# Kernel tuning notes

Hardware: AMD Instinct MI355X
Metric: run time of the kernel (lower is better)

## Reference

```python
import jax, jax.numpy as jnp
import numpy as np

N_NODES = 50000
N_EDGES = 800000
D_IN = 96
D_OUT = 96
K_ORDER = 3


def setup_inputs() -> dict:
    key = jax.random.key(0)
    k1, k2, k3, k4, k5 = jax.random.split(key, 5)
    rows = jax.random.randint(k1, (N_EDGES,), 0, N_NODES, dtype=jnp.int64 if jax.config.jax_enable_x64 else jnp.int32)
    cols = jax.random.randint(k2, (N_EDGES,), 0, N_NODES, dtype=jnp.int64 if jax.config.jax_enable_x64 else jnp.int32)
    vals = jax.random.uniform(k3, (N_EDGES,), dtype=jnp.float32) * (1.0 / 16.0)  # ~sym-normalized weights
    H = jax.random.normal(k4, (N_NODES, D_IN), dtype=jnp.float32)
    W = jax.random.normal(k5, (D_IN, D_OUT), dtype=jnp.float32) * (1.0 / np.sqrt(D_IN))
    bias = jnp.zeros((D_OUT,), dtype=jnp.float32)
    return {"rows": rows, "cols": cols, "vals": vals, "H": H, "W": W, "bias": bias}


def reference(rows, cols, vals, H, W, bias):
    n = H.shape[0]

    def spmm(X):  # L @ X via gather-multiply-scatter over COO edges
        return jax.ops.segment_sum(vals[:, None] * X[cols], rows, num_segments=n)

    def ln_mm(X):  # (2L - I) @ X
        return 2.0 * spmm(X) - X

    # k = 0 term: T_0 = H
    H_out = H @ W
    # k = 1 term: T_1 = (2L - I) H  (differentiable, as in torch code)
    T_prev = H
    T_curr = ln_mm(H)
    H_out = H_out + T_curr @ W
    # k >= 2: recurrence computed under no_grad in the original -> stop_gradient
    for _ in range(2, K_ORDER + 1):
        T_next = jax.lax.stop_gradient(2.0 * ln_mm(T_curr) - T_prev)
        H_out = H_out + T_next @ W
        T_prev, T_curr = T_curr, T_next
    return H_out + bias
```

## Files before the change

### kernel.cpp

```cpp
#include <hip/hip_runtime.h>
#include <hip/hip_fp16.h>

#define NN 50000
#define NE 800000
#define D  96
#define NB_SCAN 196
#define N4 (NN * D / 4)
#define CB4 ((N4 + 255) / 256)
#define WFRAG_BLKS 5
#define EMAX (NE + 8 * NN)
#define EZ4  (EMAX / 4)
#define EZB  ((EZ4 + 255) / 256)

typedef unsigned int   uint32;
typedef unsigned short uint16;
typedef short  v8s __attribute__((ext_vector_type(8)));
typedef float  v4f __attribute__((ext_vector_type(4)));
typedef unsigned int v2u __attribute__((ext_vector_type(2)));
typedef unsigned int v4u __attribute__((ext_vector_type(4)));

__device__ inline uint16 f32_to_bf16(float f) {
    uint32 u = __float_as_uint(f);
    u += 0x7FFF + ((u >> 16) & 1);
    return (uint16)(u >> 16);
}

__device__ inline void u2f(v2u u, float& a, float& b, float& c, float& d) {
    a = __uint_as_float(u.x << 16);
    b = __uint_as_float(u.x & 0xFFFF0000u);
    c = __uint_as_float(u.y << 16);
    d = __uint_as_float(u.y & 0xFFFF0000u);
}

__device__ inline float f16_val(uint32 e) {
    __half_raw h; h.x = (uint16)(e >> 16);
    return __half2float(__half(h));
}

__device__ inline uint32 comb2(uint32 u1, uint32 u2, uint32 u3) {
    float a1 = __uint_as_float(u1 << 16), b1 = __uint_as_float(u1 & 0xFFFF0000u);
    float a2 = __uint_as_float(u2 << 16), b2 = __uint_as_float(u2 & 0xFFFF0000u);
    float a3 = __uint_as_float(u3 << 16), b3 = __uint_as_float(u3 & 0xFFFF0000u);
    float sa = 12.f * a1 - 40.f * a2 + 32.f * a3;
    float sb = 12.f * b1 - 40.f * b2 + 32.f * b3;
    return (uint32)f32_to_bf16(sa) | ((uint32)f32_to_bf16(sb) << 16);
}

__global__ void prep(const float4* __restrict__ H, ushort4* __restrict__ Hb,
                     const float* __restrict__ W, uint16* __restrict__ Wfrag,
                     int* __restrict__ counts, v4u* __restrict__ edges4) {
    int b = blockIdx.x;
    int t = threadIdx.x;
    if (b < CB4) {
        int i = b * 256 + t;
        if (i < N4) {
            float4 v = H[i];
            ushort4 o;
            o.x = f32_to_bf16(v.x); o.y = f32_to_bf16(v.y);
            o.z = f32_to_bf16(v.z); o.w = f32_to_bf16(v.w);
            Hb[i] = o;
        }
    } else if (b < CB4 + NB_SCAN) {
        int i = (b - CB4) * 256 + t;
        if (i < NN) counts[i] = 0;
    } else if (b < CB4 + NB_SCAN + WFRAG_BLKS) {
        int idx = (b - CB4 - NB_SCAN) * 256 + t;
        if (idx < 18 * 64) {
            int bt = idx >> 6, lane = idx & 63;
            int nt = bt / 3, kc = bt % 3;
            int col = nt * 16 + (lane & 15);
            int kbase = kc * 32 + (lane >> 4) * 8;
            uint16 tmp[8];
            #pragma unroll
            for (int j = 0; j < 8; ++j) tmp[j] = f32_to_bf16(W[(kbase + j) * D + col]);
            uint32* dst = (uint32*)(Wfrag + ((size_t)bt * 64 + lane) * 8);
            const uint32* src = (const uint32*)tmp;
            #pragma unroll
            for (int j = 0; j < 4; ++j) dst[j] = src[j];
        }
    } else {
        int i = (b - CB4 - NB_SCAN - WFRAG_BLKS) * 256 + t;
        if (i < EZ4) edges4[i] = (v4u){0u, 0u, 0u, 0u};
    }
}

__global__ void hist_slots(const int* __restrict__ rows, int* __restrict__ counts,
                           int* __restrict__ slot) {
    int e = blockIdx.x * blockDim.x + threadIdx.x;
    if (e < NE) slot[e] = atomicAdd(&counts[rows[e]], 1);
}

__global__ void scan_p1(const int* __restrict__ counts, int* __restrict__ partials) {
    __shared__ int red[256];
    int t = threadIdx.x;
    int i = blockIdx.x * 256 + t;
    red[t] = (i < NN) ? ((counts[i] + 7) & ~7) : 0;
    __syncthreads();
    for (int off = 128; off > 0; off >>= 1) {
        if (t < off) red[t] += red[t + off];
        __syncthreads();
    }
    if (t == 0) partials[blockIdx.x] = red[0];
}

__global__ void scan_p23(const int* __restrict__ counts, const int* __restrict__ partials,
                         int* __restrict__ row_ptr) {
    __shared__ int pp[256];
    __shared__ int sh[256];
    int t = threadIdx.x;
    pp[t] = (t < NB_SCAN) ? partials[t] : 0;
    __syncthreads();
    for (int off = 1; off < 256; off <<= 1) {
        int u = (t >= off) ? pp[t - off] : 0;
        __syncthreads();
        pp[t] += u;
        __syncthreads();
    }
    int blk_off = (blockIdx.x == 0) ? 0 : pp[blockIdx.x - 1];
    int i = blockIdx.x * 256 + t;
    int v = (i < NN) ? ((counts[i] + 7) & ~7) : 0;
    sh[t] = v;
    __syncthreads();
    for (int off = 1; off < 256; off <<= 1) {
        int u = (t >= off) ? sh[t - off] : 0;
        __syncthreads();
        sh[t] += u;
        __syncthreads();
    }
    int excl = sh[t] - v + blk_off;
    if (i < NN) row_ptr[i] = excl;
    if (i == NN - 1) row_ptr[NN] = excl + v;
}

__global__ void fill_edges(const int* __restrict__ rows, const int* __restrict__ cols,
                           const float* __restrict__ vals, const int* __restrict__ row_ptr,
                           const int* __restrict__ slot, uint32* __restrict__ edges) {
    int e = blockIdx.x * blockDim.x + threadIdx.x;
    if (e < NE) {
        int p = row_ptr[rows[e]] + slot[e];
        __half_raw hr = __half_raw(__float2half(vals[e]));
        edges[p] = (uint32)(cols[e] & 0xFFFF) | ((uint32)hr.x << 16);
    }
}

__global__ void spmm(const int* __restrict__ row_ptr, const uint32* __restrict__ edges,
                     const uint16* __restrict__ Xb, uint16* __restrict__ Yb) {
    int tid  = threadIdx.x;
    int lane = tid & 31;
    int g    = tid >> 5;
    int r = blockIdx.x * 8 + g;
    if (r >= NN) return;
    if (lane >= 24) return;

    const v2u* xbase = (const v2u*)Xb;

    float ax = 0.f, ay = 0.f, az = 0.f, aw = 0.f;
    int s = row_ptr[r];
    int e = row_ptr[r + 1];
    for (int i = s; i < e; i += 8) {
        v4u ea = *(const v4u*)(edges + i);
        v4u eb = *(const v4u*)(edges + i + 4);
        uint32 ee[8] = {ea.x, ea.y, ea.z, ea.w, eb.x, eb.y, eb.z, eb.w};
        v2u xx[8];
        #pragma unroll
        for (int j = 0; j < 8; ++j)
            xx[j] = xbase[(size_t)(ee[j] & 0xFFFF) * 24 + lane];
        #pragma unroll
        for (int j = 0; j < 8; ++j) {
            float v = f16_val(ee[j]);
            float x0,x1,x2,x3;
            u2f(xx[j], x0,x1,x2,x3);
            ax += v*x0; ay += v*x1; az += v*x2; aw += v*x3;
        }
    }

    v2u o;
    o.x = (uint32)f32_to_bf16(ax) | ((uint32)f32_to_bf16(ay) << 16);
    o.y = (uint32)f32_to_bf16(az) | ((uint32)f32_to_bf16(aw) << 16);
    __builtin_nontemporal_store(o, (v2u*)(Yb + (size_t)r * D) + lane);
}

__global__ void mfma_gemm(const uint16* __restrict__ U1, const uint16* __restrict__ U2,
                          const uint16* __restrict__ U3, const uint16* __restrict__ Wfrag,
                          const float* __restrict__ bias, float* __restrict__ out) {
    int tid   = threadIdx.x;
    int lane  = tid & 63;
    int wv    = blockIdx.x * (blockDim.x >> 6) + (tid >> 6);
    int nwv   = gridDim.x * (blockDim.x >> 6);
    int col   = lane & 15;
    int quad  = lane >> 4;

    v8s wf[6][3];
    #pragma unroll
    for (int nt = 0; nt < 6; ++nt)
        #pragma unroll
        for (int kc = 0; kc < 3; ++kc)
            wf[nt][kc] = ((const v8s*)Wfrag)[(nt * 3 + kc) * 64 + lane];

    float bi[6];
    #pragma unroll
    for (int nt = 0; nt < 6; ++nt) bi[nt] = bias[nt * 16 + col];

    for (int s = wv; s < NN / 16; s += nwv) {
        int r0 = s * 16;
        size_t base = (size_t)(r0 + col) * D + quad * 8;
        v8s a[3];
        #pragma unroll
        for (int kc = 0; kc < 3; ++kc) {
            v4u u1 = *(const v4u*)(U1 + base + kc * 32);
            v4u u2 = *(const v4u*)(U2 + base + kc * 32);
            v4u u3 = *(const v4u*)(U3 + base + kc * 32);
            v4u sres;
            #pragma unroll
            for (int j = 0; j < 4; ++j) sres[j] = comb2(u1[j], u2[j], u3[j]);
            a[kc] = __builtin_bit_cast(v8s, sres);
        }
        v4f acc[6];
        #pragma unroll
        for (int nt = 0; nt < 6; ++nt) {
            v4f c = {0.f, 0.f, 0.f, 0.f};
            c = __builtin_amdgcn_mfma_f32_16x16x32_bf16(a[0], wf[nt][0], c, 0, 0, 0);
            c = __builtin_amdgcn_mfma_f32_16x16x32_bf16(a[1], wf[nt][1], c, 0, 0, 0);
            c = __builtin_amdgcn_mfma_f32_16x16x32_bf16(a[2], wf[nt][2], c, 0, 0, 0);
            acc[nt] = c;
        }
        #pragma unroll
        for (int nt = 0; nt < 6; ++nt) {
            float* o = out + (size_t)(r0 + quad * 4) * D + nt * 16 + col;
            __builtin_nontemporal_store(acc[nt][0] + bi[nt], o + 0 * D);
            __builtin_nontemporal_store(acc[nt][1] + bi[nt], o + 1 * D);
            __builtin_nontemporal_store(acc[nt][2] + bi[nt], o + 2 * D);
            __builtin_nontemporal_store(acc[nt][3] + bi[nt], o + 3 * D);
        }
    }
}

extern "C" void kernel_launch(void* const* d_in, const int* in_sizes, int n_in,
                              void* d_out, int out_size, void* d_ws, size_t ws_size,
                              hipStream_t stream) {
    const int*   rows = (const int*)d_in[0];
    const int*   cols = (const int*)d_in[1];
    const float* vals = (const float*)d_in[2];
    const float* H    = (const float*)d_in[3];
    const float* W    = (const float*)d_in[4];
    const float* bias = (const float*)d_in[5];
    float* out = (float*)d_out;

    char* ws = (char*)d_ws;
    uint16* Hb       = (uint16*)ws;  ws += (size_t)NN * D * 2;
    uint16* U1b      = (uint16*)ws;  ws += (size_t)NN * D * 2;
    uint16* U2b      = (uint16*)ws;  ws += (size_t)NN * D * 2;
    uint16* U3b      = (uint16*)ws;  ws += (size_t)NN * D * 2;
    uint32* edges    = (uint32*)ws;  ws += (size_t)EMAX * 4;
    uint16* Wfrag    = (uint16*)ws;  ws += (size_t)18 * 64 * 8 * 2;
    int*    counts   = (int*)ws;     ws += (size_t)NN * 4;
    int*    row_ptr  = (int*)ws;     ws += (size_t)(NN + 1) * 4;
    int*    partials = (int*)ws;     ws += 256 * 4;
    int*    slot     = (int*)U2b;

    const int eb = (NE + 255) / 256;

    prep<<<CB4 + NB_SCAN + WFRAG_BLKS + EZB, 256, 0, stream>>>(
        (const float4*)H, (ushort4*)Hb, W, Wfrag, counts, (v4u*)edges);
    hist_slots<<<eb, 256, 0, stream>>>(rows, counts, slot);
    scan_p1<<<NB_SCAN, 256, 0, stream>>>(counts, partials);
    scan_p23<<<NB_SCAN, 256, 0, stream>>>(counts, partials, row_ptr);
    fill_edges<<<eb, 256, 0, stream>>>(rows, cols, vals, row_ptr, slot, edges);

    const int sb = (NN + 7) / 8;

    spmm<<<sb, 256, 0, stream>>>(row_ptr, edges, Hb,  U1b);
    spmm<<<sb, 256, 0, stream>>>(row_ptr, edges, U1b, U2b);
    spmm<<<sb, 256, 0, stream>>>(row_ptr, edges, U2b, U3b);
    mfma_gemm<<<782, 256, 0, stream>>>(U1b, U2b, U3b, Wfrag, bias, out);
}
```

Before: 230.9 us.

## Fuse Chebyshev combination into last SpMM, unroll gather to 16, vectorize edge setup

The final SpMM now applies the 12/-40/32 linear combination of U1, U2 and its own result in the epilogue and writes a single combined matrix. The GEMM then reads one bf16 input instead of three and drops its per-element combine arithmetic. The SpMM inner loop also processes 16 edges per iteration to put more gathers in flight, and the histogram and fill kernels handle two edges per thread with vector loads. The 16-wide unroll raises register pressure, which could lower occupancy in the SpMM kernels.

```diff
diff --git a/kernel.cpp b/kernel.cpp
--- a/kernel.cpp
+++ b/kernel.cpp
@@ -18,6 +18,7 @@
 typedef float  v4f __attribute__((ext_vector_type(4)));
 typedef unsigned int v2u __attribute__((ext_vector_type(2)));
 typedef unsigned int v4u __attribute__((ext_vector_type(4)));
+typedef float v2f __attribute__((ext_vector_type(2)));
 
 __device__ inline uint16 f32_to_bf16(float f) {
     uint32 u = __float_as_uint(f);
@@ -35,15 +36,6 @@
 __device__ inline float f16_val(uint32 e) {
     __half_raw h; h.x = (uint16)(e >> 16);
     return __half2float(__half(h));
-}
-
-__device__ inline uint32 comb2(uint32 u1, uint32 u2, uint32 u3) {
-    float a1 = __uint_as_float(u1 << 16), b1 = __uint_as_float(u1 & 0xFFFF0000u);
-    float a2 = __uint_as_float(u2 << 16), b2 = __uint_as_float(u2 & 0xFFFF0000u);
-    float a3 = __uint_as_float(u3 << 16), b3 = __uint_as_float(u3 & 0xFFFF0000u);
-    float sa = 12.f * a1 - 40.f * a2 + 32.f * a3;
-    float sb = 12.f * b1 - 40.f * b2 + 32.f * b3;
-    return (uint32)f32_to_bf16(sa) | ((uint32)f32_to_bf16(sb) << 16);
 }
 
 __global__ void prep(const float4* __restrict__ H, ushort4* __restrict__ Hb,
@@ -86,8 +78,12 @@
 
 __global__ void hist_slots(const int* __restrict__ rows, int* __restrict__ counts,
                            int* __restrict__ slot) {
-    int e = blockIdx.x * blockDim.x + threadIdx.x;
-    if (e < NE) slot[e] = atomicAdd(&counts[rows[e]], 1);
+    int base = (blockIdx.x * blockDim.x + threadIdx.x) * 2;
+    if (base < NE) {
+        v2u rr = *(const v2u*)(rows + base);
+        slot[base]     = atomicAdd(&counts[rr.x], 1);
+        slot[base + 1] = atomicAdd(&counts[rr.y], 1);
+    }
 }
 
 __global__ void scan_p1(const int* __restrict__ counts, int* __restrict__ partials) {
@@ -135,11 +131,16 @@
 __global__ void fill_edges(const int* __restrict__ rows, const int* __restrict__ cols,
                            const float* __restrict__ vals, const int* __restrict__ row_ptr,
                            const int* __restrict__ slot, uint32* __restrict__ edges) {
-    int e = blockIdx.x * blockDim.x + threadIdx.x;
-    if (e < NE) {
-        int p = row_ptr[rows[e]] + slot[e];
-        __half_raw hr = __half_raw(__float2half(vals[e]));
-        edges[p] = (uint32)(cols[e] & 0xFFFF) | ((uint32)hr.x << 16);
+    int base = (blockIdx.x * blockDim.x + threadIdx.x) * 2;
+    if (base < NE) {
+        v2u rr = *(const v2u*)(rows + base);
+        v2u cc = *(const v2u*)(cols + base);
+        v2f vv = *(const v2f*)(vals + base);
+        v2u ss = *(const v2u*)(slot + base);
+        __half_raw h0 = __half_raw(__float2half(vv.x));
+        __half_raw h1 = __half_raw(__float2half(vv.y));
+        edges[row_ptr[rr.x] + ss.x] = (cc.x & 0xFFFF) | ((uint32)h0.x << 16);
+        edges[row_ptr[rr.y] + ss.y] = (cc.y & 0xFFFF) | ((uint32)h1.x << 16);
     }
 }
 
@@ -157,7 +158,27 @@
     float ax = 0.f, ay = 0.f, az = 0.f, aw = 0.f;
     int s = row_ptr[r];
     int e = row_ptr[r + 1];
-    for (int i = s; i < e; i += 8) {
+    int i = s;
+    for (; i + 15 < e; i += 16) {
+        v4u e0 = *(const v4u*)(edges + i);
+        v4u e1 = *(const v4u*)(edges + i + 4);
+        v4u e2 = *(const v4u*)(edges + i + 8);
+        v4u e3 = *(const v4u*)(edges + i + 12);
+        uint32 ee[16] = {e0.x,e0.y,e0.z,e0.w, e1.x,e1.y,e1.z,e1.w,
+                         e2.x,e2.y,e2.z,e2.w, e3.x,e3.y,e3.z,e3.w};
+        v2u xx[16];
+        #pragma unroll
+        for (int j = 0; j < 16; ++j)
+            xx[j] = xbase[(size_t)(ee[j] & 0xFFFF) * 24 + lane];
+        #pragma unroll
+        for (int j = 0; j < 16; ++j) {
+            float v = f16_val(ee[j]);
+            float x0,x1,x2,x3;
+            u2f(xx[j], x0,x1,x2,x3);
+            ax += v*x0; ay += v*x1; az += v*x2; aw += v*x3;
+        }
+    }
+    for (; i < e; i += 8) {
         v4u ea = *(const v4u*)(edges + i);
         v4u eb = *(const v4u*)(edges + i + 4);
         uint32 ee[8] = {ea.x, ea.y, ea.z, ea.w, eb.x, eb.y, eb.z, eb.w};
@@ -180,8 +201,75 @@
     __builtin_nontemporal_store(o, (v2u*)(Yb + (size_t)r * D) + lane);
 }
 
-__global__ void mfma_gemm(const uint16* __restrict__ U1, const uint16* __restrict__ U2,
-                          const uint16* __restrict__ U3, const uint16* __restrict__ Wfrag,
+__global__ void spmm_fuse(const int* __restrict__ row_ptr, const uint32* __restrict__ edges,
+                          const uint16* __restrict__ U1, const uint16* __restrict__ U2,
+                          uint16* __restrict__ Sb) {
+    int tid  = threadIdx.x;
+    int lane = tid & 31;
+    int g    = tid >> 5;
+    int r = blockIdx.x * 8 + g;
+    if (r >= NN) return;
+    if (lane >= 24) return;
+
+    const v2u* xbase = (const v2u*)U2;
+
+    float ax = 0.f, ay = 0.f, az = 0.f, aw = 0.f;
+    int s = row_ptr[r];
+    int e = row_ptr[r + 1];
+    int i = s;
+    for (; i + 15 < e; i += 16) {
+        v4u e0 = *(const v4u*)(edges + i);
+        v4u e1 = *(const v4u*)(edges + i + 4);
+        v4u e2 = *(const v4u*)(edges + i + 8);
+        v4u e3 = *(const v4u*)(edges + i + 12);
+        uint32 ee[16] = {e0.x,e0.y,e0.z,e0.w, e1.x,e1.y,e1.z,e1.w,
+                         e2.x,e2.y,e2.z,e2.w, e3.x,e3.y,e3.z,e3.w};
+        v2u xx[16];
+        #pragma unroll
+        for (int j = 0; j < 16; ++j)
+            xx[j] = xbase[(size_t)(ee[j] & 0xFFFF) * 24 + lane];
+        #pragma unroll
+        for (int j = 0; j < 16; ++j) {
+            float v = f16_val(ee[j]);
+            float x0,x1,x2,x3;
+            u2f(xx[j], x0,x1,x2,x3);
+            ax += v*x0; ay += v*x1; az += v*x2; aw += v*x3;
+        }
+    }
+    for (; i < e; i += 8) {
+        v4u ea = *(const v4u*)(edges + i);
+        v4u eb = *(const v4u*)(edges + i + 4);
+        uint32 ee[8] = {ea.x, ea.y, ea.z, ea.w, eb.x, eb.y, eb.z, eb.w};
+        v2u xx[8];
+        #pragma unroll
+        for (int j = 0; j < 8; ++j)
+            xx[j] = xbase[(size_t)(ee[j] & 0xFFFF) * 24 + lane];
+        #pragma unroll
+        for (int j = 0; j < 8; ++j) {
+            float v = f16_val(ee[j]);
+            float x0,x1,x2,x3;
+            u2f(xx[j], x0,x1,x2,x3);
+            ax += v*x0; ay += v*x1; az += v*x2; aw += v*x3;
+        }
+    }
+
+    v2u u1 = __builtin_nontemporal_load((const v2u*)(U1 + (size_t)r * D) + lane);
+    v2u u2 = xbase[(size_t)r * 24 + lane];
+    float p0,p1,p2,p3, q0,q1,q2,q3;
+    u2f(u1, p0,p1,p2,p3);
+    u2f(u2, q0,q1,q2,q3);
+    float s0 = 12.f*p0 - 40.f*q0 + 32.f*ax;
+    float s1 = 12.f*p1 - 40.f*q1 + 32.f*ay;
+    float s2 = 12.f*p2 - 40.f*q2 + 32.f*az;
+    float s3 = 12.f*p3 - 40.f*q3 + 32.f*aw;
+
+    v2u o;
+    o.x = (uint32)f32_to_bf16(s0) | ((uint32)f32_to_bf16(s1) << 16);
+    o.y = (uint32)f32_to_bf16(s2) | ((uint32)f32_to_bf16(s3) << 16);
+    __builtin_nontemporal_store(o, (v2u*)(Sb + (size_t)r * D) + lane);
+}
+
+__global__ void mfma_gemm(const uint16* __restrict__ Sb, const uint16* __restrict__ Wfrag,
                           const float* __restrict__ bias, float* __restrict__ out) {
     int tid   = threadIdx.x;
     int lane  = tid & 63;
@@ -203,25 +291,17 @@
 
     for (int s = wv; s < NN / 16; s += nwv) {
         int r0 = s * 16;
-        size_t base = (size_t)(r0 + col) * D + quad * 8;
-        v8s a[3];
-        #pragma unroll
-        for (int kc = 0; kc < 3; ++kc) {
-            v4u u1 = *(const v4u*)(U1 + base + kc * 32);
-            v4u u2 = *(const v4u*)(U2 + base + kc * 32);
-            v4u u3 = *(const v4u*)(U3 + base + kc * 32);
-            v4u sres;
-            #pragma unroll
-            for (int j = 0; j < 4; ++j) sres[j] = comb2(u1[j], u2[j], u3[j]);
-            a[kc] = __builtin_bit_cast(v8s, sres);
-        }
+        const uint16* arow = Sb + (size_t)(r0 + col) * D + quad * 8;
+        v8s a0 = *((const v8s*)(arow));
+        v8s a1 = *((const v8s*)(arow + 32));
+        v8s a2 = *((const v8s*)(arow + 64));
         v4f acc[6];
         #pragma unroll
         for (int nt = 0; nt < 6; ++nt) {
             v4f c = {0.f, 0.f, 0.f, 0.f};
-            c = __builtin_amdgcn_mfma_f32_16x16x32_bf16(a[0], wf[nt][0], c, 0, 0, 0);
-            c = __builtin_amdgcn_mfma_f32_16x16x32_bf16(a[1], wf[nt][1], c, 0, 0, 0);
-            c = __builtin_amdgcn_mfma_f32_16x16x32_bf16(a[2], wf[nt][2], c, 0, 0, 0);
+            c = __builtin_amdgcn_mfma_f32_16x16x32_bf16(a0, wf[nt][0], c, 0, 0, 0);
+            c = __builtin_amdgcn_mfma_f32_16x16x32_bf16(a1, wf[nt][1], c, 0, 0, 0);
+            c = __builtin_amdgcn_mfma_f32_16x16x32_bf16(a2, wf[nt][2], c, 0, 0, 0);
             acc[nt] = c;
         }
         #pragma unroll
@@ -250,7 +330,7 @@
     uint16* Hb       = (uint16*)ws;  ws += (size_t)NN * D * 2;
     uint16* U1b      = (uint16*)ws;  ws += (size_t)NN * D * 2;
     uint16* U2b      = (uint16*)ws;  ws += (size_t)NN * D * 2;
-    uint16* U3b      = (uint16*)ws;  ws += (size_t)NN * D * 2;
+    uint16* Sb       = (uint16*)ws;  ws += (size_t)NN * D * 2;
     uint32* edges    = (uint32*)ws;  ws += (size_t)EMAX * 4;
     uint16* Wfrag    = (uint16*)ws;  ws += (size_t)18 * 64 * 8 * 2;
     int*    counts   = (int*)ws;     ws += (size_t)NN * 4;
@@ -258,19 +338,19 @@
     int*    partials = (int*)ws;     ws += 256 * 4;
     int*    slot     = (int*)U2b;
 
-    const int eb = (NE + 255) / 256;
+    const int eb2 = (NE / 2 + 255) / 256;
 
     prep<<<CB4 + NB_SCAN + WFRAG_BLKS + EZB, 256, 0, stream>>>(
         (const float4*)H, (ushort4*)Hb, W, Wfrag, counts, (v4u*)edges);
-    hist_slots<<<eb, 256, 0, stream>>>(rows, counts, slot);
+    hist_slots<<<eb2, 256, 0, stream>>>(rows, counts, slot);
     scan_p1<<<NB_SCAN, 256, 0, stream>>>(counts, partials);
     scan_p23<<<NB_SCAN, 256, 0, stream>>>(counts, partials, row_ptr);
-    fill_edges<<<eb, 256, 0, stream>>>(rows, cols, vals, row_ptr, slot, edges);
+    fill_edges<<<eb2, 256, 0, stream>>>(rows, cols, vals, row_ptr, slot, edges);
 
     const int sb = (NN + 7) / 8;
 
     spmm<<<sb, 256, 0, stream>>>(row_ptr, edges, Hb,  U1b);
     spmm<<<sb, 256, 0, stream>>>(row_ptr, edges, U1b, U2b);
-    spmm<<<sb, 256, 0, stream>>>(row_ptr, edges, U2b, U3b);
-    mfma_gemm<<<782, 256, 0, stream>>>(U1b, U2b, U3b, Wfrag, bias, out);
-}
+    spmm_fuse<<<sb, 256, 0, stream>>>(row_ptr, edges, U1b, U2b, Sb);
+    mfma_gemm<<<782, 256, 0, stream>>>(Sb, Wfrag, bias, out);
+}
```

New measurement: 229.9 us. No clear change (-0.4%).
